# Optimization experiments

Hardware: AMD Instinct MI355X
Metric: run time of the kernel (lower is better)

The kernel has to match this reference:

```python
import jax, jax.numpy as jnp
import numpy as np
from jax import lax

jax.config.update("jax_enable_x64", True)  # source casts distances to double for sinkhorn

N_E = 512
E_DIM = 256
NUM_EXPERTS = 10
B = 8192
MU = 0.25
BETA = 1.0
SK_EPS = 0.01
SK_ITERS = 100


def setup_inputs() -> dict:
    key = jax.random.key(0)
    k0, k1, k2, k3 = jax.random.split(key, 4)
    x = jax.random.normal(k0, (B, E_DIM), dtype=jnp.float32)
    label = jax.random.randint(k1, (N_E,), 0, 10)  # cluster id per code of codebook 0
    gate_probs = jax.random.uniform(k2, (B, NUM_EXPERTS), dtype=jnp.float32)
    # embeddings initialized uniform(-1/n_e, 1/n_e) as in __init__
    emb = jax.random.uniform(k3, (NUM_EXPERTS + 1, N_E, E_DIM), dtype=jnp.float32,
                             minval=-1.0 / N_E, maxval=1.0 / N_E)
    return {"x": x, "label": label, "idx": 0, "gate_probs": gate_probs, "emb": emb}


def _sinkhorn(d, eps, iters):
    # standard SwAV-style sinkhorn (as used in UniTok/LETTER); d: [B, K] float64
    logits = -d / eps
    Q = jnp.exp(logits - jnp.max(logits))  # max-shift is a no-op after global normalization
    Q = (Q / jnp.sum(Q)).T  # [K, B]
    K, Bn = Q.shape

    def step(Q, _):
        Q = Q / (jnp.sum(Q, axis=1, keepdims=True) * K)
        Q = Q / (jnp.sum(Q, axis=0, keepdims=True) * Bn)
        return Q, None

    Q, _ = lax.scan(step, Q, None, length=iters)
    return (Q * Bn).T  # [B, K]


def _assign(latent, W):
    d = (jnp.sum(latent ** 2, axis=1, keepdims=True)
         + jnp.sum(W ** 2, axis=1)[None, :]
         - 2.0 * latent @ W.T)  # [B, n_e]
    mx, mn = jnp.max(d), jnp.min(d)
    mid = (mx + mn) / 2
    amp = mx - mid + 1e-5
    d = ((d - mid) / amp).astype(jnp.float64)
    Q = _sinkhorn(d, SK_EPS, SK_ITERS)
    return jnp.argmax(Q, axis=-1)  # [B]


def reference(x, label, idx, gate_probs, emb):
    latent = x.reshape(-1, E_DIM)  # [B, D]
    nb = latent.shape[0]

    # per-expert sinkhorn assignment (use_sk=True, sk_epsilon>0 path)
    indices_all = jax.vmap(lambda W: _assign(latent, W))(emb)          # [11, B]
    xq_all = jax.vmap(lambda W, i: W[i])(emb, indices_all)              # [11, B, D]

    x_q = jnp.einsum('be,ebd->bd', gate_probs, xq_all[:NUM_EXPERTS])
    x_q = 0.95 * x_q + 0.05 * xq_all[NUM_EXPERTS]

    # diversity loss on codebook 0: positive = another code in the same cluster
    ind0 = indices_all[0]                      # [B]
    clusters = label[ind0]                     # [B]
    ar = jnp.arange(N_E)
    pos_mask = (label[None, :] == clusters[:, None]) & (ar[None, :] != ind0[:, None])
    y_true = jnp.argmax(pos_mask, axis=1)      # deterministic positive sample
    sim = x_q @ emb[0].T                       # [B, n_e]
    sim = sim.at[jnp.arange(nb), ind0].add(-1e12)  # mask self-similarity
    logp = jax.nn.log_softmax(sim, axis=-1)
    diversity_loss = -jnp.mean(logp[jnp.arange(nb), y_true])

    commitment_loss = jnp.mean((lax.stop_gradient(x_q) - x) ** 2)
    codebook_loss = jnp.mean((x_q - lax.stop_gradient(x)) ** 2)
    loss = codebook_loss + MU * commitment_loss + BETA * diversity_loss

    # selected index per token: codebook of top expert
    expert_id = jnp.argmax(gate_probs, axis=1)          # [B] in [0,10)
    indices = indices_all.T[jnp.arange(nb), expert_id]  # [B]

    x_q_out = x + lax.stop_gradient(x_q - x)  # straight-through
    return x_q_out, loss, indices
```

## Files before the change

kernel.cpp:

```cpp
#include <hip/hip_runtime.h>
#include <cstdint>
#include <cstddef>

#define NTOK 8192
#define NE 512
#define EDIM 256
#define NEXPALL 11
#define NITER 100

static __device__ __forceinline__ double wredsum(double x) {
  for (int o = 32; o > 0; o >>= 1) x += __shfl_down(x, o, 64);
  return x;
}

static constexpr double S32 = 2.3283064365386963e-10;
static constexpr double Q32 = 4294967296.0;

__global__ void k_init(unsigned* colmin, double* r0, double* r1, double* uprev,
                       unsigned* dmaxA, unsigned* dminA, int* conv_iter, double* sums) {
  int i = blockIdx.x * 256 + threadIdx.x;
  if (i < NEXPALL * NTOK) colmin[i] = 0x7F800000u;
  if (i < NEXPALL * NE) { r0[i] = 0.0; r1[i] = 0.0; uprev[i] = 0.0; }
  if (i < NEXPALL) { dmaxA[i] = 0u; dminA[i] = 0x7F800000u; conv_iter[i] = 1 << 30; }
  if (i < 2) sums[i] = 0.0;
}

__global__ __launch_bounds__(256) void k_npsq(const float* __restrict__ p, float* __restrict__ o, int rows) {
  int r = blockIdx.x * 16 + (threadIdx.x >> 4);
  int l = threadIdx.x & 15;
  if (r >= rows) return;
  const float* a = p + (size_t)r * EDIM;
  int leaf = l >> 3;
  int j = l & 7;
  const float* base = a + leaf * 128 + j;
  float acc = __fmul_rn(base[0], base[0]);
#pragma unroll
  for (int i = 8; i < 128; i += 8) {
    float v = base[i];
    acc = __fadd_rn(acc, __fmul_rn(v, v));
  }
  acc = __fadd_rn(acc, __shfl_xor(acc, 1, 64));
  acc = __fadd_rn(acc, __shfl_xor(acc, 2, 64));
  acc = __fadd_rn(acc, __shfl_xor(acc, 4, 64));
  float other = __shfl_xor(acc, 8, 64);
  float tot = (leaf == 0) ? __fadd_rn(acc, other) : __fadd_rn(other, acc);
  if (l == 0) o[r] = tot;
}

__global__ __launch_bounds__(256, 2) void k_gemm_d(const float* __restrict__ x, const float* __restrict__ emb,
                                                   const float* __restrict__ sx, const float* __restrict__ sw,
                                                   float* __restrict__ bigF,
                                                   unsigned* __restrict__ colminA,
                                                   unsigned* __restrict__ dmaxA,
                                                   unsigned* __restrict__ dminA) {
  int bx = blockIdx.x, by = blockIdx.y, e = blockIdx.z;
  int tid = threadIdx.x;
  int tx = tid & 15, ty = tid >> 4;
  int b0 = bx * 128, k0 = by * 128;

  __shared__ float xs[16][128];
  __shared__ float es[16][128];
  __shared__ float sxs[128];
  __shared__ float sws[128];
  __shared__ unsigned colm[128];
  __shared__ float wrx[4], wrn[4];

  if (tid < 128) { sxs[tid] = sx[b0 + tid]; colm[tid] = 0x7F800000u; }
  else { sws[tid - 128] = sw[e * NE + k0 + tid - 128]; }

  int lr = tid & 127;
  int lh = tid >> 7;
  const float* xrow = x + (size_t)(b0 + lr) * EDIM + lh * 8;
  const float* wrow = emb + ((size_t)e * NE + k0 + lr) * EDIM + lh * 8;

  float4 xa = *(const float4*)(xrow + 0);
  float4 xb = *(const float4*)(xrow + 4);
  float4 wa = *(const float4*)(wrow + 0);
  float4 wb = *(const float4*)(wrow + 4);

  float acc[8][8] = {};

  for (int kc = 0; kc < EDIM; kc += 16) {
    __syncthreads();
    xs[lh * 8 + 0][lr] = xa.x; xs[lh * 8 + 1][lr] = xa.y;
    xs[lh * 8 + 2][lr] = xa.z; xs[lh * 8 + 3][lr] = xa.w;
    xs[lh * 8 + 4][lr] = xb.x; xs[lh * 8 + 5][lr] = xb.y;
    xs[lh * 8 + 6][lr] = xb.z; xs[lh * 8 + 7][lr] = xb.w;
    es[lh * 8 + 0][lr] = wa.x; es[lh * 8 + 1][lr] = wa.y;
    es[lh * 8 + 2][lr] = wa.z; es[lh * 8 + 3][lr] = wa.w;
    es[lh * 8 + 4][lr] = wb.x; es[lh * 8 + 5][lr] = wb.y;
    es[lh * 8 + 6][lr] = wb.z; es[lh * 8 + 7][lr] = wb.w;
    __syncthreads();
    if (kc + 16 < EDIM) {
      xa = *(const float4*)(xrow + kc + 16);
      xb = *(const float4*)(xrow + kc + 20);
      wa = *(const float4*)(wrow + kc + 16);
      wb = *(const float4*)(wrow + kc + 20);
    }
#pragma unroll
    for (int kk = 0; kk < 16; ++kk) {
      float4 xv0 = *(const float4*)&xs[kk][tx * 4];
      float4 xv1 = *(const float4*)&xs[kk][64 + tx * 4];
      float4 wv0 = *(const float4*)&es[kk][ty * 4];
      float4 wv1 = *(const float4*)&es[kk][64 + ty * 4];
      float xr[8] = {xv0.x, xv0.y, xv0.z, xv0.w, xv1.x, xv1.y, xv1.z, xv1.w};
      float wr[8] = {wv0.x, wv0.y, wv0.z, wv0.w, wv1.x, wv1.y, wv1.z, wv1.w};
#pragma unroll
      for (int i = 0; i < 8; ++i)
#pragma unroll
        for (int j = 0; j < 8; ++j)
          acc[i][j] = fmaf(xr[i], wr[j], acc[i][j]);
    }
  }

  float dmx = -3.0e38f, dmn = 3.0e38f;
#pragma unroll
  for (int i = 0; i < 8; ++i) {
    int tokL = (i >> 2) * 64 + tx * 4 + (i & 3);
    float sxv = sxs[tokL];
    float cmin = 3.0e38f;
#pragma unroll
    for (int j = 0; j < 8; ++j) {
      int codeL = (j >> 2) * 64 + ty * 4 + (j & 3);
      float m2 = __fmul_rn(2.0f, acc[i][j]);
      float dv = __fsub_rn(__fadd_rn(sxv, sws[codeL]), m2);
      acc[i][j] = dv;
      dmx = fmaxf(dmx, dv); dmn = fminf(dmn, dv);
      cmin = fminf(cmin, dv);
    }
    atomicMin(&colm[tokL], __float_as_uint(cmin));
  }
  for (int o = 32; o > 0; o >>= 1) {
    dmx = fmaxf(dmx, __shfl_down(dmx, o, 64));
    dmn = fminf(dmn, __shfl_down(dmn, o, 64));
  }
  int wvi = tid >> 6, ln = tid & 63;
  if (ln == 0) { wrx[wvi] = dmx; wrn[wvi] = dmn; }
  __syncthreads();
  if (tid == 0) {
    float m1 = fmaxf(fmaxf(wrx[0], wrx[1]), fmaxf(wrx[2], wrx[3]));
    float m2 = fminf(fminf(wrn[0], wrn[1]), fminf(wrn[2], wrn[3]));
    atomicMax(dmaxA + e, __float_as_uint(m1));
    atomicMin(dminA + e, __float_as_uint(m2));
  }
  if (tid < 128) atomicMin(colminA + (size_t)e * NTOK + b0 + tid, colm[tid]);
#pragma unroll
  for (int j2 = 0; j2 < 2; ++j2)
#pragma unroll
    for (int cc = 0; cc < 4; ++cc) {
      int code = j2 * 64 + ty * 4 + cc;
      int cj = j2 * 4 + cc;
      float* ob = bigF + ((size_t)e * NE + k0 + code) * NTOK + b0;
      float4 lo = make_float4(acc[0][cj], acc[1][cj], acc[2][cj], acc[3][cj]);
      float4 hi = make_float4(acc[4][cj], acc[5][cj], acc[6][cj], acc[7][cj]);
      *(float4*)(ob + tx * 4) = lo;
      *(float4*)(ob + 64 + tx * 4) = hi;
    }
}

__global__ __launch_bounds__(256) void k_prep(const unsigned* __restrict__ colminA,
                                              const unsigned* __restrict__ dmaxA,
                                              const unsigned* __restrict__ dminA,
                                              double* __restrict__ cml, double* __restrict__ v) {
  int e = blockIdx.y;
  int b = blockIdx.x * 256 + threadIdx.x;
  float mx = __uint_as_float(dmaxA[e]);
  float mn = __uint_as_float(dminA[e]);
  float mid = __fmul_rn(__fadd_rn(mx, mn), 0.5f);
  float amp = __fadd_rn(__fsub_rn(mx, mid), 1e-5f);
  float cminf = __uint_as_float(colminA[(size_t)e * NTOK + b]);
  float dn = __fdiv_rn(__fsub_rn(cminf, mid), amp);
  double l = (-(double)dn) / 0.01;
  cml[(size_t)e * NTOK + b] = l;
  v[(size_t)e * NTOK + b] = exp(l);
}

__global__ __launch_bounds__(256) void k_build(float* __restrict__ bigF,
                                               const unsigned* __restrict__ dmaxA,
                                               const unsigned* __restrict__ dminA,
                                               const double* __restrict__ cml, const double* __restrict__ v0,
                                               double* __restrict__ r0) {
  int bx = blockIdx.x, k = blockIdx.y, e = blockIdx.z;
  int tid = threadIdx.x;
  float mx = __uint_as_float(dmaxA[e]);
  float mn = __uint_as_float(dminA[e]);
  float mid = __fmul_rn(__fadd_rn(mx, mn), 0.5f);
  float amp = __fadd_rn(__fsub_rn(mx, mid), 1e-5f);
  size_t rb = ((size_t)e * NE + k) * NTOK;
  int cb = bx * 2048 + tid * 8;
  float4 fa = *(const float4*)(bigF + rb + cb);
  float4 fb = *(const float4*)(bigF + rb + cb + 4);
  float din[8] = {fa.x, fa.y, fa.z, fa.w, fb.x, fb.y, fb.z, fb.w};
  unsigned qo[8];
  double racc = 0.0;
#pragma unroll
  for (int j = 0; j < 8; ++j) {
    int b = cb + j;
    float dn = __fdiv_rn(__fsub_rn(din[j], mid), amp);
    double l = (-(double)dn) / 0.01;
    double t = l - cml[(size_t)e * NTOK + b];
    double Bv = exp(t);
    double qd = (1.0 - Bv) * Q32;
    qd = fmin(fmax(qd, 0.0), 4294967295.0);
    unsigned q = (unsigned)llrint(qd);
    qo[j] = q;
    double Bq = fma(-(double)q, S32, 1.0);
    racc = fma(Bq, v0[(size_t)e * NTOK + b], racc);
  }
  uint4 oa = make_uint4(qo[0], qo[1], qo[2], qo[3]);
  uint4 ob2 = make_uint4(qo[4], qo[5], qo[6], qo[7]);
  *(uint4*)((unsigned*)bigF + rb + cb) = oa;
  *(uint4*)((unsigned*)bigF + rb + cb + 4) = ob2;
  racc = wredsum(racc);
  __shared__ double pr[4];
  int wv = tid >> 6, ln = tid & 63;
  if (ln == 0) pr[wv] = racc;
  __syncthreads();
  if (tid == 0) atomicAdd(&r0[e * NE + k], (pr[0] + pr[1]) + (pr[2] + pr[3]));
}

__global__ __launch_bounds__(256) void k_iter_a(const unsigned* __restrict__ bigU,
                                                const double* __restrict__ rc, double* __restrict__ rn,
                                                double* __restrict__ v, double* __restrict__ uprev,
                                                int* conv_iter, int t) {
  int e = blockIdx.y, bx = blockIdx.x, tid = threadIdx.x;
  int ci = ((volatile int*)conv_iter)[e];
  if (t > ci) {
    if (bx == 0) {
      int k2 = tid * 2;
      rn[e * NE + k2] = rc[e * NE + k2];
      rn[e * NE + k2 + 1] = rc[e * NE + k2 + 1];
    }
    return;
  }
  __shared__ double us[NE];
  __shared__ int okf;
  if (tid == 0) okf = 1;
  int k2 = tid * 2;
  double u0 = 1.0 / (512.0 * rc[e * NE + k2]);
  double u1 = 1.0 / (512.0 * rc[e * NE + k2 + 1]);
  us[k2] = u0; us[k2 + 1] = u1;
  __syncthreads();
  if (bx == 0) {
    double p0 = uprev[e * NE + k2], p1 = uprev[e * NE + k2 + 1];
    bool ok = (fabs(u0 - p0) <= 1e-13 * fabs(u0)) && (fabs(u1 - p1) <= 1e-13 * fabs(u1));
    if (!ok) okf = 0;
    uprev[e * NE + k2] = u0; uprev[e * NE + k2 + 1] = u1;
    rn[e * NE + k2] = 0.0; rn[e * NE + k2 + 1] = 0.0;
  }
  __syncthreads();
  if (bx == 0 && tid == 0 && okf) atomicMin(conv_iter + e, t);

  int col = bx * 256 + tid;
  const unsigned* cp = bigU + (size_t)e * NE * NTOK + col;
  double c0 = 0, c1 = 0, c2 = 0, c3 = 0;
#pragma unroll 2
  for (int k = 0; k < NE; k += 4) {
    unsigned q0 = cp[(size_t)(k + 0) * NTOK];
    unsigned q1 = cp[(size_t)(k + 1) * NTOK];
    unsigned q2 = cp[(size_t)(k + 2) * NTOK];
    unsigned q3 = cp[(size_t)(k + 3) * NTOK];
    c0 = fma(us[k + 0], fma(-(double)q0, S32, 1.0), c0);
    c1 = fma(us[k + 1], fma(-(double)q1, S32, 1.0), c1);
    c2 = fma(us[k + 2], fma(-(double)q2, S32, 1.0), c2);
    c3 = fma(us[k + 3], fma(-(double)q3, S32, 1.0), c3);
  }
  double c = (c0 + c1) + (c2 + c3);
  v[(size_t)e * NTOK + col] = 1.0 / (8192.0 * c);
}

__global__ __launch_bounds__(256) void k_iter_b(const unsigned* __restrict__ bigU,
                                                const double* __restrict__ v, double* __restrict__ rn,
                                                const int* conv_iter, int t) {
  int e = blockIdx.z;
  if (t > ((volatile int*)conv_iter)[e]) return;
  int bx = blockIdx.x, ky = blockIdx.y, tid = threadIdx.x;
  int wv = tid >> 6, ln = tid & 63;
  int cb = bx * 2048 + tid * 8;
  const double* vb = v + (size_t)e * NTOK + cb;
  double v0 = vb[0], v1 = vb[1], v2 = vb[2], v3 = vb[3];
  double v4 = vb[4], v5 = vb[5], v6 = vb[6], v7 = vb[7];
  __shared__ double part[16][4];
  size_t ebase = (size_t)e * NE * NTOK;
  for (int rr = 0; rr < 4; ++rr) {
#pragma unroll 4
    for (int kk = 0; kk < 16; ++kk) {
      int k = ky * 64 + rr * 16 + kk;
      const unsigned* rp = bigU + ebase + (size_t)k * NTOK + cb;
      uint4 qa = *(const uint4*)rp;
      uint4 qb = *(const uint4*)(rp + 4);
      double p;
      p = v0 * fma(-(double)qa.x, S32, 1.0);
      p = fma(v1, fma(-(double)qa.y, S32, 1.0), p);
      p = fma(v2, fma(-(double)qa.z, S32, 1.0), p);
      p = fma(v3, fma(-(double)qa.w, S32, 1.0), p);
      p = fma(v4, fma(-(double)qb.x, S32, 1.0), p);
      p = fma(v5, fma(-(double)qb.y, S32, 1.0), p);
      p = fma(v6, fma(-(double)qb.z, S32, 1.0), p);
      p = fma(v7, fma(-(double)qb.w, S32, 1.0), p);
      p = wredsum(p);
      if (ln == 0) part[kk][wv] = p;
    }
    __syncthreads();
    if (tid < 16)
      atomicAdd(&rn[e * NE + ky * 64 + rr * 16 + tid],
                (part[tid][0] + part[tid][1]) + (part[tid][2] + part[tid][3]));
    __syncthreads();
  }
}

__global__ __launch_bounds__(256) void k_final(const unsigned* __restrict__ bigU,
                                               const double* __restrict__ rfin, int* __restrict__ idxs) {
  int e = blockIdx.y, bx = blockIdx.x, tid = threadIdx.x;
  __shared__ double us[NE];
  int k2 = tid * 2;
  us[k2] = 1.0 / (512.0 * rfin[e * NE + k2]);
  us[k2 + 1] = 1.0 / (512.0 * rfin[e * NE + k2 + 1]);
  __syncthreads();
  int col = bx * 256 + tid;
  const unsigned* cp = bigU + (size_t)e * NE * NTOK + col;
  double best = -1.0;
  int bi = 0;
#pragma unroll 4
  for (int k = 0; k < NE; ++k) {
    double s = us[k] * fma(-(double)cp[(size_t)k * NTOK], S32, 1.0);
    if (s > best) { best = s; bi = k; }
  }
  idxs[(size_t)e * NTOK + col] = bi;
}

__global__ __launch_bounds__(256) void k_mix(const float* __restrict__ x, const float* __restrict__ gate,
                                             const float* __restrict__ emb, const int* __restrict__ idxs,
                                             float* __restrict__ xq, float* __restrict__ out0,
                                             float* __restrict__ outIdx, double* __restrict__ mse_sum) {
  int tid = threadIdx.x;
  int sub = tid >> 5, lane = tid & 31;
  int tok = blockIdx.x * 8 + sub;
  float acc[8] = {0, 0, 0, 0, 0, 0, 0, 0};
#pragma unroll
  for (int ee = 0; ee < 10; ++ee) {
    int id = idxs[(size_t)ee * NTOK + tok];
    float g = gate[tok * 10 + ee];
    const float* er = emb + ((size_t)ee * NE + id) * EDIM + lane;
#pragma unroll
    for (int dd = 0; dd < 8; ++dd) acc[dd] = fmaf(g, er[32 * dd], acc[dd]);
  }
  int id10 = idxs[(size_t)10 * NTOK + tok];
  const float* es = emb + ((size_t)10 * NE + id10) * EDIM + lane;
  double ms = 0.0;
#pragma unroll
  for (int dd = 0; dd < 8; ++dd) {
    int d = lane + 32 * dd;
    float q = 0.95f * acc[dd] + 0.05f * es[32 * dd];
    float xv = x[(size_t)tok * EDIM + d];
    float df = q - xv;
    out0[(size_t)tok * EDIM + d] = xv + df;
    xq[(size_t)tok * EDIM + d] = q;
    ms += (double)df * (double)df;
  }
  ms = wredsum(ms);
  __shared__ double pr[4];
  int wv = tid >> 6, ln = tid & 63;
  if (ln == 0) pr[wv] = ms;
  __syncthreads();
  if (tid == 0) atomicAdd(mse_sum, (pr[0] + pr[1]) + (pr[2] + pr[3]));
  if (lane == 0) {
    const float* gr = gate + tok * 10;
    float bg = gr[0];
    int be = 0;
#pragma unroll
    for (int ee = 1; ee < 10; ++ee) { float g = gr[ee]; if (g > bg) { bg = g; be = ee; } }
    outIdx[tok] = (float)idxs[(size_t)be * NTOK + tok];
  }
}

__global__ __launch_bounds__(256, 2) void k_simgemm(const float* __restrict__ xq, const float* __restrict__ emb,
                                                    float* __restrict__ sim) {
  int bx = blockIdx.x, by = blockIdx.y, tid = threadIdx.x;
  int tx = tid & 15, ty = tid >> 4;
  int b0 = bx * 128, j0 = by * 128;
  __shared__ float xs[16][128];
  __shared__ float es[16][128];
  int lr = tid & 127;
  int lh = tid >> 7;
  const float* xrow = xq + (size_t)(b0 + lr) * EDIM + lh * 8;
  const float* erow = emb + (size_t)(j0 + lr) * EDIM + lh * 8;
  float4 xa = *(const float4*)(xrow + 0);
  float4 xb = *(const float4*)(xrow + 4);
  float4 wa = *(const float4*)(erow + 0);
  float4 wb = *(const float4*)(erow + 4);
  float acc[8][8] = {};
  for (int kc = 0; kc < EDIM; kc += 16) {
    __syncthreads();
    xs[lh * 8 + 0][lr] = xa.x; xs[lh * 8 + 1][lr] = xa.y;
    xs[lh * 8 + 2][lr] = xa.z; xs[lh * 8 + 3][lr] = xa.w;
    xs[lh * 8 + 4][lr] = xb.x; xs[lh * 8 + 5][lr] = xb.y;
    xs[lh * 8 + 6][lr] = xb.z; xs[lh * 8 + 7][lr] = xb.w;
    es[lh * 8 + 0][lr] = wa.x; es[lh * 8 + 1][lr] = wa.y;
    es[lh * 8 + 2][lr] = wa.z; es[lh * 8 + 3][lr] = wa.w;
    es[lh * 8 + 4][lr] = wb.x; es[lh * 8 + 5][lr] = wb.y;
    es[lh * 8 + 6][lr] = wb.z; es[lh * 8 + 7][lr] = wb.w;
    __syncthreads();
    if (kc + 16 < EDIM) {
      xa = *(const float4*)(xrow + kc + 16);
      xb = *(const float4*)(xrow + kc + 20);
      wa = *(const float4*)(erow + kc + 16);
      wb = *(const float4*)(erow + kc + 20);
    }
#pragma unroll
    for (int kk = 0; kk < 16; ++kk) {
      float4 xv0 = *(const float4*)&xs[kk][ty * 4];
      float4 xv1 = *(const float4*)&xs[kk][64 + ty * 4];
      float4 wv0 = *(const float4*)&es[kk][tx * 4];
      float4 wv1 = *(const float4*)&es[kk][64 + tx * 4];
      float xr[8] = {xv0.x, xv0.y, xv0.z, xv0.w, xv1.x, xv1.y, xv1.z, xv1.w};
      float wr[8] = {wv0.x, wv0.y, wv0.z, wv0.w, wv1.x, wv1.y, wv1.z, wv1.w};
#pragma unroll
      for (int i = 0; i < 8; ++i)
#pragma unroll
        for (int j = 0; j < 8; ++j)
          acc[i][j] = fmaf(xr[i], wr[j], acc[i][j]);
    }
  }
#pragma unroll
  for (int i = 0; i < 8; ++i) {
    int tok = (i >> 2) * 64 + ty * 4 + (i & 3);
    float* ob = sim + (size_t)(b0 + tok) * NE + j0;
    float4 lo = make_float4(acc[i][0], acc[i][1], acc[i][2], acc[i][3]);
    float4 hi = make_float4(acc[i][4], acc[i][5], acc[i][6], acc[i][7]);
    *(float4*)(ob + tx * 4) = lo;
    *(float4*)(ob + 64 + tx * 4) = hi;
  }
}

__global__ __launch_bounds__(256) void k_div(const float* __restrict__ sim, const int* __restrict__ idxs,
                                             const int* __restrict__ label, double* __restrict__ div_sum) {
  __shared__ int lab[NE];
  int tid = threadIdx.x;
  lab[tid] = label[tid];
  lab[256 + tid] = label[256 + tid];
  __syncthreads();
  int wv = tid >> 6, ln = tid & 63;
  int b = blockIdx.x * 4 + wv;
  int ind0 = idxs[b];
  int clu = lab[ind0];
  const float* sr = sim + (size_t)b * NE;
  double vals[8];
  double mx = -1e300;
  int ys = 1024;
#pragma unroll
  for (int c = 0; c < 8; ++c) {
    int j = ln + 64 * c;
    double vv = (double)sr[j];
    if (j == ind0) vv -= 1e12;
    vals[c] = vv;
    mx = fmax(mx, vv);
    if (lab[j] == clu && j != ind0 && j < ys) ys = j;
  }
  for (int o = 32; o > 0; o >>= 1) {
    mx = fmax(mx, __shfl_xor(mx, o, 64));
    ys = min(ys, __shfl_xor(ys, o, 64));
  }
  int y = (ys >= 1024) ? 0 : ys;
  double se = 0.0, vy = 0.0;
#pragma unroll
  for (int c = 0; c < 8; ++c) {
    int j = ln + 64 * c;
    se += exp(vals[c] - mx);
    if (j == y) vy = vals[c];
  }
  for (int o = 32; o > 0; o >>= 1) {
    se += __shfl_xor(se, o, 64);
    vy += __shfl_xor(vy, o, 64);
  }
  if (ln == 0) {
    double lse = mx + log(se);
    atomicAdd(div_sum, lse - vy);
  }
}

__global__ void k_loss(const double* __restrict__ sums, float* __restrict__ out) {
  double mse = sums[0] / 2097152.0;
  double dv = sums[1] / 8192.0;
  double loss = (mse + 0.25 * mse) + dv;
  out[0] = (float)loss;
}

extern "C" void kernel_launch(void* const* d_in, const int* in_sizes, int n_in,
                              void* d_out, int out_size, void* d_ws, size_t ws_size,
                              hipStream_t stream) {
  (void)in_sizes; (void)n_in; (void)out_size;
  const float* x = (const float*)d_in[0];
  const int* label = (const int*)d_in[1];
  const float* gate = (const float*)d_in[3];
  const float* emb = (const float*)d_in[4];
  float* out = (float*)d_out;
  float* out0 = out;
  float* outLoss = out + (size_t)NTOK * EDIM;
  float* outIdx = out + (size_t)NTOK * EDIM + 1;

  char* w = (char*)d_ws;
  size_t off = 0;
  auto alloc = [&](size_t bytes) -> void* {
    void* p = w + off;
    off += (bytes + 15) & ~(size_t)15;
    return p;
  };
  float* bigF = (float*)alloc((size_t)NEXPALL * NE * NTOK * 4);
  unsigned* bigU = (unsigned*)bigF;
  float* sim = (float*)bigF;
  unsigned* colminA = (unsigned*)alloc((size_t)NEXPALL * NTOK * 4);
  double* cml = (double*)alloc((size_t)NEXPALL * NTOK * 8);
  double* v = (double*)alloc((size_t)NEXPALL * NTOK * 8);
  double* r0 = (double*)alloc((size_t)NEXPALL * NE * 8);
  double* r1 = (double*)alloc((size_t)NEXPALL * NE * 8);
  double* uprev = (double*)alloc((size_t)NEXPALL * NE * 8);
  float* sxF = (float*)alloc((size_t)NTOK * 4);
  float* swF = (float*)alloc((size_t)NEXPALL * NE * 4);
  unsigned* dmaxA = (unsigned*)alloc(NEXPALL * 4);
  unsigned* dminA = (unsigned*)alloc(NEXPALL * 4);
  int* conv_iter = (int*)alloc(NEXPALL * 4);
  int* idxs = (int*)alloc((size_t)NEXPALL * NTOK * 4);
  float* xq = (float*)alloc((size_t)NTOK * EDIM * 4);
  double* sums = (double*)alloc(2 * 8);
  if (off > ws_size) return;

  k_init<<<352, 256, 0, stream>>>(colminA, r0, r1, uprev, dmaxA, dminA, conv_iter, sums);
  k_npsq<<<NTOK / 16, 256, 0, stream>>>(x, sxF, NTOK);
  k_npsq<<<(NEXPALL * NE) / 16, 256, 0, stream>>>(emb, swF, NEXPALL * NE);
  k_gemm_d<<<dim3(64, 4, NEXPALL), 256, 0, stream>>>(x, emb, sxF, swF, bigF, colminA, dmaxA, dminA);
  k_prep<<<dim3(32, NEXPALL), 256, 0, stream>>>(colminA, dmaxA, dminA, cml, v);
  k_build<<<dim3(4, NE, NEXPALL), 256, 0, stream>>>(bigF, dmaxA, dminA, cml, v, r0);
  for (int t = 1; t <= NITER; ++t) {
    const double* rc = (t & 1) ? r0 : r1;
    double* rn = (t & 1) ? r1 : r0;
    k_iter_a<<<dim3(32, NEXPALL), 256, 0, stream>>>(bigU, rc, rn, v, uprev, conv_iter, t);
    k_iter_b<<<dim3(4, 8, NEXPALL), 256, 0, stream>>>(bigU, v, rn, conv_iter, t);
  }
  k_final<<<dim3(32, NEXPALL), 256, 0, stream>>>(bigU, r1, idxs);
  k_mix<<<NTOK / 8, 256, 0, stream>>>(x, gate, emb, idxs, xq, out0, outIdx, sums);
  k_simgemm<<<dim3(64, 4), 256, 0, stream>>>(xq, emb, sim);
  k_div<<<NTOK / 4, 256, 0, stream>>>(sim, idxs, label, sums + 1);
  k_loss<<<1, 1, 0, stream>>>(sums, outLoss);
}
```

Before: 1.341 ms.

## Fuse Sinkhorn column and row passes into one kernel with per-block partial sums

The two per-iteration Sinkhorn kernels are merged into one. Each block computes the column scalings for its 256 tokens, keeps them in shared memory, and then immediately computes partial row sums over those same columns. The partials go to a per-block buffer without atomics and are reduced at the start of the next iteration. This halves the launch count and rereads each block's slice of the quantized matrix while it is likely still in cache, at the cost of a 32-way partial reduction per iteration. Separately, the launch bounds of the two GEMM kernels are raised from 2 to 4 blocks per SM, which may increase register pressure.

```diff
diff --git a/kernel.cpp b/kernel.cpp
--- a/kernel.cpp
+++ b/kernel.cpp
@@ -16,11 +16,11 @@
 static constexpr double S32 = 2.3283064365386963e-10;
 static constexpr double Q32 = 4294967296.0;
 
-__global__ void k_init(unsigned* colmin, double* r0, double* r1, double* uprev,
+__global__ void k_init(unsigned* colmin, double* r0, double* uprev,
                        unsigned* dmaxA, unsigned* dminA, int* conv_iter, double* sums) {
   int i = blockIdx.x * 256 + threadIdx.x;
   if (i < NEXPALL * NTOK) colmin[i] = 0x7F800000u;
-  if (i < NEXPALL * NE) { r0[i] = 0.0; r1[i] = 0.0; uprev[i] = 0.0; }
+  if (i < NEXPALL * NE) { r0[i] = 0.0; uprev[i] = 0.0; }
   if (i < NEXPALL) { dmaxA[i] = 0u; dminA[i] = 0x7F800000u; conv_iter[i] = 1 << 30; }
   if (i < 2) sums[i] = 0.0;
 }
@@ -47,7 +47,7 @@
   if (l == 0) o[r] = tot;
 }
 
-__global__ __launch_bounds__(256, 2) void k_gemm_d(const float* __restrict__ x, const float* __restrict__ emb,
+__global__ __launch_bounds__(256, 4) void k_gemm_d(const float* __restrict__ x, const float* __restrict__ emb,
                                                    const float* __restrict__ sx, const float* __restrict__ sw,
                                                    float* __restrict__ bigF,
                                                    unsigned* __restrict__ colminA,
@@ -219,40 +219,48 @@
   if (tid == 0) atomicAdd(&r0[e * NE + k], (pr[0] + pr[1]) + (pr[2] + pr[3]));
 }
 
-__global__ __launch_bounds__(256) void k_iter_a(const unsigned* __restrict__ bigU,
-                                                const double* __restrict__ rc, double* __restrict__ rn,
-                                                double* __restrict__ v, double* __restrict__ uprev,
-                                                int* conv_iter, int t) {
-  int e = blockIdx.y, bx = blockIdx.x, tid = threadIdx.x;
-  int ci = ((volatile int*)conv_iter)[e];
-  if (t > ci) {
-    if (bx == 0) {
-      int k2 = tid * 2;
-      rn[e * NE + k2] = rc[e * NE + k2];
-      rn[e * NE + k2 + 1] = rc[e * NE + k2 + 1];
-    }
-    return;
-  }
+__global__ __launch_bounds__(256) void k_iter_f(const unsigned* __restrict__ bigU,
+                                                const double* __restrict__ r0,
+                                                double* __restrict__ rpart,
+                                                double* __restrict__ uprev,
+                                                int* __restrict__ conv_iter, int t) {
+  int e = blockIdx.y, sub = blockIdx.x, tid = threadIdx.x;
+  if (t > ((volatile int*)conv_iter)[e]) return;
   __shared__ double us[NE];
+  __shared__ double vloc[256];
   __shared__ int okf;
   if (tid == 0) okf = 1;
+  size_t ebase = (size_t)e * NE * NTOK;
+  const double* rp_e = rpart + (size_t)e * 32 * NE;
+  double* rp_mine = rpart + ((size_t)e * 32 + sub) * NE;
+
   int k2 = tid * 2;
-  double u0 = 1.0 / (512.0 * rc[e * NE + k2]);
-  double u1 = 1.0 / (512.0 * rc[e * NE + k2 + 1]);
+  double s0, s1;
+  if (t == 1) {
+    s0 = r0[e * NE + k2];
+    s1 = r0[e * NE + k2 + 1];
+  } else {
+    s0 = 0.0; s1 = 0.0;
+    for (int j = 0; j < 32; ++j) {
+      s0 += rp_e[(size_t)j * NE + k2];
+      s1 += rp_e[(size_t)j * NE + k2 + 1];
+    }
+  }
+  double u0 = 1.0 / (512.0 * s0);
+  double u1 = 1.0 / (512.0 * s1);
   us[k2] = u0; us[k2 + 1] = u1;
   __syncthreads();
-  if (bx == 0) {
+  if (sub == 0) {
     double p0 = uprev[e * NE + k2], p1 = uprev[e * NE + k2 + 1];
     bool ok = (fabs(u0 - p0) <= 1e-13 * fabs(u0)) && (fabs(u1 - p1) <= 1e-13 * fabs(u1));
     if (!ok) okf = 0;
     uprev[e * NE + k2] = u0; uprev[e * NE + k2 + 1] = u1;
-    rn[e * NE + k2] = 0.0; rn[e * NE + k2 + 1] = 0.0;
-  }
-  __syncthreads();
-  if (bx == 0 && tid == 0 && okf) atomicMin(conv_iter + e, t);
-
-  int col = bx * 256 + tid;
-  const unsigned* cp = bigU + (size_t)e * NE * NTOK + col;
+  }
+  __syncthreads();
+  if (sub == 0 && tid == 0 && okf) atomicMin(conv_iter + e, t);
+
+  int col = sub * 256 + tid;
+  const unsigned* cp = bigU + ebase + col;
   double c0 = 0, c1 = 0, c2 = 0, c3 = 0;
 #pragma unroll 2
   for (int k = 0; k < NE; k += 4) {
@@ -266,58 +274,42 @@
     c3 = fma(us[k + 3], fma(-(double)q3, S32, 1.0), c3);
   }
   double c = (c0 + c1) + (c2 + c3);
-  v[(size_t)e * NTOK + col] = 1.0 / (8192.0 * c);
-}
-
-__global__ __launch_bounds__(256) void k_iter_b(const unsigned* __restrict__ bigU,
-                                                const double* __restrict__ v, double* __restrict__ rn,
-                                                const int* conv_iter, int t) {
-  int e = blockIdx.z;
-  if (t > ((volatile int*)conv_iter)[e]) return;
-  int bx = blockIdx.x, ky = blockIdx.y, tid = threadIdx.x;
+  vloc[tid] = 1.0 / (8192.0 * c);
+  __syncthreads();
+
   int wv = tid >> 6, ln = tid & 63;
-  int cb = bx * 2048 + tid * 8;
-  const double* vb = v + (size_t)e * NTOK + cb;
-  double v0 = vb[0], v1 = vb[1], v2 = vb[2], v3 = vb[3];
-  double v4 = vb[4], v5 = vb[5], v6 = vb[6], v7 = vb[7];
-  __shared__ double part[16][4];
-  size_t ebase = (size_t)e * NE * NTOK;
-  for (int rr = 0; rr < 4; ++rr) {
-#pragma unroll 4
-    for (int kk = 0; kk < 16; ++kk) {
-      int k = ky * 64 + rr * 16 + kk;
-      const unsigned* rp = bigU + ebase + (size_t)k * NTOK + cb;
-      uint4 qa = *(const uint4*)rp;
-      uint4 qb = *(const uint4*)(rp + 4);
-      double p;
-      p = v0 * fma(-(double)qa.x, S32, 1.0);
-      p = fma(v1, fma(-(double)qa.y, S32, 1.0), p);
-      p = fma(v2, fma(-(double)qa.z, S32, 1.0), p);
-      p = fma(v3, fma(-(double)qa.w, S32, 1.0), p);
-      p = fma(v4, fma(-(double)qb.x, S32, 1.0), p);
-      p = fma(v5, fma(-(double)qb.y, S32, 1.0), p);
-      p = fma(v6, fma(-(double)qb.z, S32, 1.0), p);
-      p = fma(v7, fma(-(double)qb.w, S32, 1.0), p);
-      p = wredsum(p);
-      if (ln == 0) part[kk][wv] = p;
-    }
-    __syncthreads();
-    if (tid < 16)
-      atomicAdd(&rn[e * NE + ky * 64 + rr * 16 + tid],
-                (part[tid][0] + part[tid][1]) + (part[tid][2] + part[tid][3]));
-    __syncthreads();
+  int cb = sub * 256 + ln * 4;
+  double vv0 = vloc[ln * 4 + 0], vv1 = vloc[ln * 4 + 1];
+  double vv2 = vloc[ln * 4 + 2], vv3 = vloc[ln * 4 + 3];
+  for (int k = wv; k < NE; k += 4) {
+    const unsigned* rp = bigU + ebase + (size_t)k * NTOK + cb;
+    uint4 qa = *(const uint4*)rp;
+    double p;
+    p = vv0 * fma(-(double)qa.x, S32, 1.0);
+    p = fma(vv1, fma(-(double)qa.y, S32, 1.0), p);
+    p = fma(vv2, fma(-(double)qa.z, S32, 1.0), p);
+    p = fma(vv3, fma(-(double)qa.w, S32, 1.0), p);
+    p = wredsum(p);
+    if (ln == 0) rp_mine[k] = p;
   }
 }
 
 __global__ __launch_bounds__(256) void k_final(const unsigned* __restrict__ bigU,
-                                               const double* __restrict__ rfin, int* __restrict__ idxs) {
-  int e = blockIdx.y, bx = blockIdx.x, tid = threadIdx.x;
+                                               const double* __restrict__ rpart,
+                                               int* __restrict__ idxs) {
+  int e = blockIdx.y, sub = blockIdx.x, tid = threadIdx.x;
   __shared__ double us[NE];
+  const double* rp_e = rpart + (size_t)e * 32 * NE;
   int k2 = tid * 2;
-  us[k2] = 1.0 / (512.0 * rfin[e * NE + k2]);
-  us[k2 + 1] = 1.0 / (512.0 * rfin[e * NE + k2 + 1]);
-  __syncthreads();
-  int col = bx * 256 + tid;
+  double s0 = 0.0, s1 = 0.0;
+  for (int j = 0; j < 32; ++j) {
+    s0 += rp_e[(size_t)j * NE + k2];
+    s1 += rp_e[(size_t)j * NE + k2 + 1];
+  }
+  us[k2] = 1.0 / (512.0 * s0);
+  us[k2 + 1] = 1.0 / (512.0 * s1);
+  __syncthreads();
+  int col = sub * 256 + tid;
   const unsigned* cp = bigU + (size_t)e * NE * NTOK + col;
   double best = -1.0;
   int bi = 0;
@@ -374,7 +366,7 @@
   }
 }
 
-__global__ __launch_bounds__(256, 2) void k_simgemm(const float* __restrict__ xq, const float* __restrict__ emb,
+__global__ __launch_bounds__(256, 4) void k_simgemm(const float* __restrict__ xq, const float* __restrict__ emb,
                                                     float* __restrict__ sim) {
   int bx = blockIdx.x, by = blockIdx.y, tid = threadIdx.x;
   int tx = tid & 15, ty = tid >> 4;
@@ -513,7 +505,7 @@
   double* cml = (double*)alloc((size_t)NEXPALL * NTOK * 8);
   double* v = (double*)alloc((size_t)NEXPALL * NTOK * 8);
   double* r0 = (double*)alloc((size_t)NEXPALL * NE * 8);
-  double* r1 = (double*)alloc((size_t)NEXPALL * NE * 8);
+  double* rpart = (double*)alloc((size_t)NEXPALL * 32 * NE * 8);
   double* uprev = (double*)alloc((size_t)NEXPALL * NE * 8);
   float* sxF = (float*)alloc((size_t)NTOK * 4);
   float* swF = (float*)alloc((size_t)NEXPALL * NE * 4);
@@ -525,19 +517,15 @@
   double* sums = (double*)alloc(2 * 8);
   if (off > ws_size) return;
 
-  k_init<<<352, 256, 0, stream>>>(colminA, r0, r1, uprev, dmaxA, dminA, conv_iter, sums);
+  k_init<<<352, 256, 0, stream>>>(colminA, r0, uprev, dmaxA, dminA, conv_iter, sums);
   k_npsq<<<NTOK / 16, 256, 0, stream>>>(x, sxF, NTOK);
   k_npsq<<<(NEXPALL * NE) / 16, 256, 0, stream>>>(emb, swF, NEXPALL * NE);
   k_gemm_d<<<dim3(64, 4, NEXPALL), 256, 0, stream>>>(x, emb, sxF, swF, bigF, colminA, dmaxA, dminA);
   k_prep<<<dim3(32, NEXPALL), 256, 0, stream>>>(colminA, dmaxA, dminA, cml, v);
   k_build<<<dim3(4, NE, NEXPALL), 256, 0, stream>>>(bigF, dmaxA, dminA, cml, v, r0);
-  for (int t = 1; t <= NITER; ++t) {
-    const double* rc = (t & 1) ? r0 : r1;
-    double* rn = (t & 1) ? r1 : r0;
-    k_iter_a<<<dim3(32, NEXPALL), 256, 0, stream>>>(bigU, rc, rn, v, uprev, conv_iter, t);
-    k_iter_b<<<dim3(4, 8, NEXPALL), 256, 0, stream>>>(bigU, v, rn, conv_iter, t);
-  }
-  k_final<<<dim3(32, NEXPALL), 256, 0, stream>>>(bigU, r1, idxs);
+  for (int t = 1; t <= NITER - 1; ++t)
+    k_iter_f<<<dim3(32, NEXPALL), 256, 0, stream>>>(bigU, r0, rpart, uprev, conv_iter, t);
+  k_final<<<dim3(32, NEXPALL), 256, 0, stream>>>(bigU, rpart, idxs);
   k_mix<<<NTOK / 8, 256, 0, stream>>>(x, gate, emb, idxs, xq, out0, outIdx, sums);
   k_simgemm<<<dim3(64, 4), 256, 0, stream>>>(xq, emb, sim);
   k_div<<<NTOK / 4, 256, 0, stream>>>(sim, idxs, label, sums + 1);
```

Result: slower. 2.184 ms (+62.9%).
